# Performance work log

Measured on AMD Instinct MI355X. Metric: run time of the kernel, lower is better.

Reference implementation:

```python
import jax, jax.numpy as jnp
import numpy as np

B, R, C_M, C_Z, H, DH, NQP = 2, 384, 384, 128, 12, 32, 4
W_C = (2.0 / (9 * NQP)) ** (-0.5)   # (2/(9*n_qp))^-0.5
W_L = 3.0 ** 0.5                     # (1/3)^-0.5


def setup_inputs() -> dict:
    key = jax.random.key(0)
    ks = jax.random.split(key, 10)
    pair_rep = jax.random.normal(ks[0], (B, R, R, C_Z), jnp.float32)
    sing_rep = jax.random.normal(ks[1], (B, R, C_M), jnp.float32)
    m = jax.random.normal(ks[2], (B, R, 3, 3), jnp.float32)
    bbr, _ = jnp.linalg.qr(m)  # orthonormal backbone frames (B,R,3,3)
    bbt = jax.random.normal(ks[3], (B, R, 3), jnp.float32)
    s = 0.02
    W_qkv = jax.random.normal(ks[4], (C_M, DH * 3 * H), jnp.float32) * s
    W_qk = jax.random.normal(ks[5], (C_M, H * 2 * NQP * 3), jnp.float32) * s
    W_fc1 = jax.random.normal(ks[6], (C_Z, H), jnp.float32) * s
    b_fc1 = jnp.zeros((H,), jnp.float32)
    W0 = jax.random.normal(ks[7], (H * DH, C_M), jnp.float32) * s
    W1 = jax.random.normal(ks[8], (H * C_Z, C_M), jnp.float32) * s
    gamma = jax.random.uniform(ks[9], (1,), jnp.float32)
    return dict(pair_rep=pair_rep, sing_rep=sing_rep, bbr=bbr, bbt=bbt,
                W_qkv=W_qkv, W_qk=W_qk, W_fc1=W_fc1, b_fc1=b_fc1,
                W0=W0, W1=W1, gamma=gamma)


def reference(pair_rep, sing_rep, bbr, bbt, W_qkv, W_qk, W_fc1, b_fc1, W0, W1, gamma):
    # pair bias: fc1 then b i j h -> b h i j
    pair_bias = jnp.transpose(jnp.einsum('bijc,ch->bijh', pair_rep, W_fc1) + b_fc1,
                              (0, 3, 1, 2))                      # b h i j
    # scalar q/k/v: channel layout (dim_head, 3, heads)
    qkv = (sing_rep @ W_qkv).reshape(B, R, DH, 3, H)
    rq, rk, rv = (jnp.transpose(qkv[:, :, :, i, :], (0, 3, 1, 2)) for i in range(3))  # b h r d
    dot = jnp.einsum('bhid,bhjd->bhij', rq, rk) * DH ** (-0.5)
    # point q/k: channel layout (heads, 2, n_qp, 3)
    qk = (sing_rep @ W_qk).reshape(B, R, H, 2, NQP, 3)
    gq = jnp.transpose(qk[:, :, :, 0], (0, 3, 1, 2, 4))          # b p r h a
    gk = jnp.transpose(qk[:, :, :, 1], (0, 3, 1, 2, 4))
    # frame-transformed query/key points
    Tq = jnp.einsum('bprha,brak->phbrk', gq, bbr) + bbt          # p h b r 3
    Tk = jnp.einsum('bprha,brak->phbrk', gk, bbr) + bbt
    diff = Tq[:, :, :, :, None, :] - Tk[:, :, :, None, :, :]     # p h b i j 3
    sq = jnp.transpose(jnp.sum(diff * diff, axis=(0, -1)), (1, 0, 2, 3))  # b h i j
    head_w = jax.nn.softplus(gamma[0]) * W_C / 2                 # same scalar per head
    attn = jax.nn.softmax(W_L * (pair_bias + dot + head_w * sq), axis=-1)
    # pair-rep value aggregation -> W_1
    top = jnp.einsum('bhij,bijc->bihc', attn, pair_rep).reshape(B, R, H * C_Z) @ W1
    # scalar value aggregation -> W_0   (note: original adds these two only;
    # the point-value 'bot' branch is computed but unused in the output)
    out = jnp.transpose(jnp.einsum('bhij,bhjd->bhid', attn, rv),
                        (0, 2, 1, 3)).reshape(B, R, H * DH) @ W0
    return out + top
```

## Files before the change

kernel.cpp:

```cpp
#include <hip/hip_runtime.h>
#include <math.h>

#define Bb   2
#define Rr   384
#define CMd  384
#define CZ   128
#define Hh   12
#define DHd  32

#define WL           1.7320508075688772f
#define WC           4.242640687119285f
#define INV_SQRT_DH  0.17677669529663687f

#define SZ_R   (Bb*Hh*Rr*DHd)
#define SZ_T   (Bb*Hh*Rr*12)
#define SZ_S   (Bb*Hh*Rr)
#define SZ_A   ((long)Bb*Hh*Rr*Rr)
#define SZ_O   (Bb*Rr*Hh*DHd)

__global__ __launch_bounds__(64) void k_projgemm(
    const float* __restrict__ sing, const float* __restrict__ Wqkv,
    const float* __restrict__ Wqk, float* __restrict__ pbuf)
{
  const int t = threadIdx.x;
  const int m0 = blockIdx.x * 32;
  const int n0 = blockIdx.y * 32;
  const int ks = blockIdx.z;
  const int tx = t & 7, ty = t >> 3;
  __shared__ float As[32][36];
  __shared__ float Bs[32][36];
  float acc[4][4] = {};

  for (int kc = ks*192; kc < ks*192 + 192; kc += 32) {
    #pragma unroll
    for (int i = 0; i < 4; ++i) {
      int s = t + 64*i;
      int row = s >> 3, k4 = (s & 7) << 2;
      float4 v = *(const float4*)(sing + (long)(m0 + row)*384 + kc + k4);
      As[k4  ][row] = v.x; As[k4+1][row] = v.y;
      As[k4+2][row] = v.z; As[k4+3][row] = v.w;
    }
    #pragma unroll
    for (int i = 0; i < 4; ++i) {
      int s = t + 64*i;
      int k = s >> 3, c4 = (s & 7) << 2;
      const float* srcB = (n0 < 1152)
          ? Wqkv + (long)(kc + k)*1152 + n0 + c4
          : Wqk  + (long)(kc + k)*288 + (n0 - 1152) + c4;
      float4 w = *(const float4*)srcB;
      Bs[k][c4] = w.x; Bs[k][c4+1] = w.y; Bs[k][c4+2] = w.z; Bs[k][c4+3] = w.w;
    }
    __syncthreads();
    #pragma unroll
    for (int k = 0; k < 32; ++k) {
      float4 a = *(const float4*)&As[k][ty*4];
      float4 b = *(const float4*)&Bs[k][tx*4];
      acc[0][0] += a.x*b.x; acc[0][1] += a.x*b.y; acc[0][2] += a.x*b.z; acc[0][3] += a.x*b.w;
      acc[1][0] += a.y*b.x; acc[1][1] += a.y*b.y; acc[1][2] += a.y*b.z; acc[1][3] += a.y*b.w;
      acc[2][0] += a.z*b.x; acc[2][1] += a.z*b.y; acc[2][2] += a.z*b.z; acc[2][3] += a.z*b.w;
      acc[3][0] += a.w*b.x; acc[3][1] += a.w*b.y; acc[3][2] += a.w*b.z; acc[3][3] += a.w*b.w;
    }
    __syncthreads();
  }
  float* pd = pbuf + (long)ks * (768*1440);
  #pragma unroll
  for (int i = 0; i < 4; ++i)
    *(float4*)&pd[(long)(m0 + ty*4 + i)*1440 + n0 + tx*4] =
        make_float4(acc[i][0], acc[i][1], acc[i][2], acc[i][3]);
}

__global__ __launch_bounds__(256) void k_scatter(
    const float* __restrict__ pbuf,
    float* __restrict__ rq, float* __restrict__ rk, float* __restrict__ rv,
    float* __restrict__ gbuf)
{
  const int idx = blockIdx.x*256 + threadIdx.x;
  const int row = idx / 360;
  const int n   = (idx - row*360) * 4;
  float4 a = ((const float4*)pbuf)[idx];
  float4 b = ((const float4*)(pbuf + (long)768*1440))[idx];
  float v[4] = {a.x + b.x, a.y + b.y, a.z + b.z, a.w + b.w};
  const int bb = row / Rr, rr = row - bb*Rr;
  #pragma unroll
  for (int j = 0; j < 4; ++j) {
    int nj = n + j;
    if (nj < 1152) {
      int d = nj/36, rem = nj - d*36, wh = rem/12, h = rem - wh*12;
      float* dst = (wh == 0) ? rq : (wh == 1) ? rk : rv;
      dst[(((long)bb*Hh + h)*Rr + rr)*DHd + d] = v[j];
    } else {
      gbuf[(long)row*288 + nj - 1152] = v[j];
    }
  }
}

__global__ __launch_bounds__(256) void k_frame(
    const float* __restrict__ gbuf, const float* __restrict__ bbr,
    const float* __restrict__ bbt,
    float* __restrict__ TqF, float* __restrict__ TkF,
    float* __restrict__ Qsq, float* __restrict__ Ksq)
{
  const int idx = blockIdx.x*256 + threadIdx.x;
  const int row = idx / 24, q = idx - row*24;
  const int h = q >> 1, s2 = q & 1;
  const float* gp = gbuf + (long)row*288 + h*24 + s2*12;
  float rot[9], tr[3];
  #pragma unroll
  for (int a = 0; a < 9; ++a) rot[a] = bbr[(long)row*9 + a];
  #pragma unroll
  for (int a = 0; a < 3; ++a) tr[a] = bbt[(long)row*3 + a];
  const int b = row / Rr, r = row - b*Rr;
  float* T = s2 ? TkF : TqF;
  const long tb = (((long)b*Hh + h)*Rr + r)*12;
  float v[12]; float ss = 0.f;
  #pragma unroll
  for (int p = 0; p < 4; ++p)
    #pragma unroll
    for (int k2 = 0; k2 < 3; ++k2) {
      float x = gp[p*3+0]*rot[k2] + gp[p*3+1]*rot[3+k2] + gp[p*3+2]*rot[6+k2] + tr[k2];
      v[p*3+k2] = x; ss += x*x;
    }
  *(float4*)(T + tb)     = make_float4(v[0], v[1], v[2],  v[3]);
  *(float4*)(T + tb + 4) = make_float4(v[4], v[5], v[6],  v[7]);
  *(float4*)(T + tb + 8) = make_float4(v[8], v[9], v[10], v[11]);
  (s2 ? Ksq : Qsq)[((long)b*Hh + h)*Rr + r] = ss;
}

__global__ __launch_bounds__(256) void k_pbias(
    const float* __restrict__ pair, const float* __restrict__ Wfc1,
    const float* __restrict__ bfc1, float* __restrict__ pb)
{
  const int t = threadIdx.x;
  const int su = t & 7, rg = t >> 3;
  __shared__ __align__(16) float w_t[12*128];
  __shared__ float bias_l[12];
  for (int s = t; s < 1536; s += 256) {
    int h = s >> 7, c = s & 127;
    w_t[s] = Wfc1[c*12 + h];
  }
  if (t < 12) bias_l[t] = bfc1[t];
  __syncthreads();

  const long rbase = (long)blockIdx.x * 128;
  const float4* pr = (const float4*)pair;
  float acc[4][12] = {};
  #pragma unroll
  for (int cc = 0; cc < 4; ++cc) {
    const int f = su + 8*cc;
    float4 p0 = pr[(rbase + rg      )*32 + f];
    float4 p1 = pr[(rbase + rg + 32 )*32 + f];
    float4 p2 = pr[(rbase + rg + 64 )*32 + f];
    float4 p3 = pr[(rbase + rg + 96 )*32 + f];
    #pragma unroll
    for (int h = 0; h < 12; ++h) {
      float4 wv = *(const float4*)&w_t[h*128 + f*4];
      acc[0][h] += p0.x*wv.x + p0.y*wv.y + p0.z*wv.z + p0.w*wv.w;
      acc[1][h] += p1.x*wv.x + p1.y*wv.y + p1.z*wv.z + p1.w*wv.w;
      acc[2][h] += p2.x*wv.x + p2.y*wv.y + p2.z*wv.z + p2.w*wv.w;
      acc[3][h] += p3.x*wv.x + p3.y*wv.y + p3.z*wv.z + p3.w*wv.w;
    }
  }
  #pragma unroll
  for (int rr = 0; rr < 4; ++rr)
    #pragma unroll
    for (int h = 0; h < 12; ++h) {
      float v = acc[rr][h];
      v += __shfl_xor(v, 1, 64);
      v += __shfl_xor(v, 2, 64);
      v += __shfl_xor(v, 4, 64);
      acc[rr][h] = v;
    }
  if (su == 0) {
    const int b0 = (int)(rbase / 147456);
    const long ro = rbase - (long)b0*147456;
    #pragma unroll
    for (int rr = 0; rr < 4; ++rr) {
      const long jrow = ro + rg + 32*rr;
      #pragma unroll
      for (int h = 0; h < 12; ++h)
        pb[((long)b0*Hh + h)*147456 + jrow] = acc[rr][h] + bias_l[h];
    }
  }
}

#define ITILE 8
__global__ __launch_bounds__(256) void k_scores(
    const float* __restrict__ rq, const float* __restrict__ rk,
    const float* __restrict__ TqF, const float* __restrict__ TkF,
    const float* __restrict__ Qsq, const float* __restrict__ Ksq,
    const float* __restrict__ gamma, float* __restrict__ attn)
{
  const int t = threadIdx.x;
  const int nt = Rr / ITILE;
  const int bh = blockIdx.x / nt;
  const int i0 = (blockIdx.x - bh*nt) * ITILE;
  __shared__ float rk_l[384][33];
  __shared__ float rq_l[32];
  __shared__ float tq_l[12];
  __shared__ float scal[1];
  __shared__ float redm[4], reds[4];

  for (int idx = t; idx < 384*32; idx += 256)
    rk_l[idx >> 5][idx & 31] = rk[(long)bh*Rr*DHd + idx];

  const float g0 = gamma[0];
  const float head_w = log1pf(__expf(g0)) * (WC * 0.5f);

  for (int ii = 0; ii < ITILE; ++ii) {
    const int i = i0 + ii;
    if (t < 32) rq_l[t] = rq[((long)bh*Rr + i)*DHd + t];
    if (t < 12) tq_l[t] = TqF[((long)bh*Rr + i)*12 + t];
    if (t == 0) scal[0] = Qsq[(long)bh*Rr + i];
    __syncthreads();
    const float qs = scal[0];
    const long rowbase = ((long)bh*Rr + i)*Rr;

    auto logit_at = [&](int j) -> float {
      float dt = 0.f;
      #pragma unroll
      for (int dd = 0; dd < 32; ++dd) dt += rq_l[dd] * rk_l[j][dd];
      const float4* tk = (const float4*)(TkF + ((long)bh*Rr + j)*12);
      float4 ta = tk[0], tb = tk[1], tc = tk[2];
      float pt = tq_l[0]*ta.x + tq_l[1]*ta.y + tq_l[2]*ta.z + tq_l[3]*ta.w
               + tq_l[4]*tb.x + tq_l[5]*tb.y + tq_l[6]*tb.z + tq_l[7]*tb.w
               + tq_l[8]*tc.x + tq_l[9]*tc.y + tq_l[10]*tc.z + tq_l[11]*tc.w;
      float sqv = qs + Ksq[(long)bh*Rr + j] - 2.f*pt;
      return WL * (attn[rowbase + j] + dt*INV_SQRT_DH + head_w*sqv);
    };

    float l0 = logit_at(t);
    float l1 = (t < 128) ? logit_at(t + 256) : -3.4e38f;
    float m = fmaxf(l0, l1);
    #pragma unroll
    for (int s = 32; s; s >>= 1) m = fmaxf(m, __shfl_xor(m, s, 64));
    if ((t & 63) == 0) redm[t >> 6] = m;
    __syncthreads();
    m = fmaxf(fmaxf(redm[0], redm[1]), fmaxf(redm[2], redm[3]));
    float e0 = __expf(l0 - m);
    float e1 = (t < 128) ? __expf(l1 - m) : 0.f;
    float s = e0 + e1;
    #pragma unroll
    for (int sh = 32; sh; sh >>= 1) s += __shfl_xor(s, sh, 64);
    if ((t & 63) == 0) reds[t >> 6] = s;
    __syncthreads();
    float inv = 1.f / (reds[0] + reds[1] + reds[2] + reds[3]);
    attn[rowbase + t] = e0 * inv;
    if (t < 128) attn[rowbase + t + 256] = e1 * inv;
    __syncthreads();
  }
}

__global__ __launch_bounds__(256) void k_agg(
    const float* __restrict__ attn, const float* __restrict__ pair,
    const float* __restrict__ rv, float* __restrict__ o_ihd, float* __restrict__ top)
{
  const int t = threadIdx.x;
  const int bi = blockIdx.x;
  const int b = bi / Rr;
  const int i = bi - b*Rr;
  __shared__ float a_l[12][384];
  for (int idx = t; idx < 12*384; idx += 256) {
    int h = idx / 384, j = idx - h*384;
    a_l[h][j] = attn[(((long)b*Hh + h)*Rr + i)*Rr + j];
  }
  __syncthreads();
  const int c = t & 127, hh = t >> 7;
  const float* prow = pair + (long)bi * Rr * CZ;
  float acc0=0,acc1=0,acc2=0,acc3=0,acc4=0,acc5=0;
  for (int j = 0; j < 384; ++j) {
    float v = prow[(long)j*CZ + c];
    acc0 += a_l[hh   ][j]*v;
    acc1 += a_l[hh+2 ][j]*v;
    acc2 += a_l[hh+4 ][j]*v;
    acc3 += a_l[hh+6 ][j]*v;
    acc4 += a_l[hh+8 ][j]*v;
    acc5 += a_l[hh+10][j]*v;
  }
  float* tp = top + ((long)bi*Hh)*CZ + c;
  tp[(long)(hh   )*CZ] = acc0;
  tp[(long)(hh+2 )*CZ] = acc1;
  tp[(long)(hh+4 )*CZ] = acc2;
  tp[(long)(hh+6 )*CZ] = acc3;
  tp[(long)(hh+8 )*CZ] = acc4;
  tp[(long)(hh+10)*CZ] = acc5;
  for (int o = t; o < 384; o += 256) {
    int h = o >> 5, dd = o & 31;
    const float* rvp = rv + ((long)b*Hh + h)*Rr*DHd + dd;
    float s = 0.f;
    for (int j = 0; j < 384; ++j) s += a_l[h][j] * rvp[(long)j*DHd];
    o_ihd[(long)bi*384 + o] = s;
  }
}

#define K5_KSPLIT 6
#define K5_KLEN   320
__global__ __launch_bounds__(64) void k_final_part(
    const float* __restrict__ o_ihd, const float* __restrict__ top,
    const float* __restrict__ W0, const float* __restrict__ W1,
    float* __restrict__ partial)
{
  const int t = threadIdx.x;
  const int m0 = blockIdx.x * 32;
  const int n0 = blockIdx.y * 32;
  const int ks = blockIdx.z;
  const int tx = t & 7, ty = t >> 3;
  __shared__ float As[32][36];
  __shared__ float Bs[32][36];
  float acc[4][4] = {};

  for (int kc = ks*K5_KLEN; kc < ks*K5_KLEN + K5_KLEN; kc += 32) {
    #pragma unroll
    for (int i = 0; i < 4; ++i) {
      int s = t + 64*i;
      int row = s >> 3, k4 = (s & 7) << 2;
      int gk = kc + k4;
      const float* srcA = (gk < 384)
          ? o_ihd + (long)(m0 + row)*384 + gk
          : top   + (long)(m0 + row)*1536 + (gk - 384);
      float4 v = *(const float4*)srcA;
      As[k4  ][row] = v.x; As[k4+1][row] = v.y;
      As[k4+2][row] = v.z; As[k4+3][row] = v.w;
    }
    #pragma unroll
    for (int i = 0; i < 4; ++i) {
      int s = t + 64*i;
      int k = s >> 3, c4 = (s & 7) << 2;
      int gk = kc + k;
      const float* srcB = (gk < 384)
          ? W0 + (long)gk*384 + n0 + c4
          : W1 + (long)(gk - 384)*384 + n0 + c4;
      float4 w = *(const float4*)srcB;
      Bs[k][c4] = w.x; Bs[k][c4+1] = w.y; Bs[k][c4+2] = w.z; Bs[k][c4+3] = w.w;
    }
    __syncthreads();
    #pragma unroll
    for (int k = 0; k < 32; ++k) {
      float4 a = *(const float4*)&As[k][ty*4];
      float4 b = *(const float4*)&Bs[k][tx*4];
      acc[0][0] += a.x*b.x; acc[0][1] += a.x*b.y; acc[0][2] += a.x*b.z; acc[0][3] += a.x*b.w;
      acc[1][0] += a.y*b.x; acc[1][1] += a.y*b.y; acc[1][2] += a.y*b.z; acc[1][3] += a.y*b.w;
      acc[2][0] += a.z*b.x; acc[2][1] += a.z*b.y; acc[2][2] += a.z*b.z; acc[2][3] += a.z*b.w;
      acc[3][0] += a.w*b.x; acc[3][1] += a.w*b.y; acc[3][2] += a.w*b.z; acc[3][3] += a.w*b.w;
    }
    __syncthreads();
  }
  float* pdst = partial + (long)ks * (768*384);
  #pragma unroll
  for (int i = 0; i < 4; ++i)
    *(float4*)&pdst[(long)(m0 + ty*4 + i)*384 + n0 + tx*4] =
        make_float4(acc[i][0], acc[i][1], acc[i][2], acc[i][3]);
}

__global__ __launch_bounds__(256) void k_final_reduce(
    const float* __restrict__ partial, float* __restrict__ out)
{
  const int idx = blockIdx.x*256 + threadIdx.x;
  float4 r = make_float4(0.f, 0.f, 0.f, 0.f);
  #pragma unroll
  for (int p = 0; p < K5_KSPLIT; ++p) {
    float4 a = ((const float4*)(partial + (long)p*768*384))[idx];
    r.x += a.x; r.y += a.y; r.z += a.z; r.w += a.w;
  }
  ((float4*)out)[idx] = r;
}

extern "C" void kernel_launch(void* const* d_in, const int* in_sizes, int n_in,
                              void* d_out, int out_size, void* d_ws, size_t ws_size,
                              hipStream_t stream)
{
  (void)in_sizes; (void)n_in; (void)out_size; (void)ws_size;
  const float* pair  = (const float*)d_in[0];
  const float* sing  = (const float*)d_in[1];
  const float* bbr   = (const float*)d_in[2];
  const float* bbt   = (const float*)d_in[3];
  const float* Wqkv  = (const float*)d_in[4];
  const float* Wqk   = (const float*)d_in[5];
  const float* Wfc1  = (const float*)d_in[6];
  const float* bfc1  = (const float*)d_in[7];
  const float* W0    = (const float*)d_in[8];
  const float* W1    = (const float*)d_in[9];
  const float* gamma = (const float*)d_in[10];
  float* out = (float*)d_out;

  float* ws    = (float*)d_ws;
  float* rq    = ws;
  float* rk    = rq  + SZ_R;
  float* rv    = rk  + SZ_R;
  float* TqF   = rv  + SZ_R;
  float* TkF   = TqF + SZ_T;
  float* Qsq   = TkF + SZ_T;
  float* Ksq   = Qsq + SZ_S;
  float* attn  = Ksq + SZ_S;
  float* o_ihd = attn + SZ_A;
  float* top   = o_ihd + SZ_O;
  float* gbuf  = o_ihd;
  float* pbuf  = attn;
  float* partial = attn;

  k_projgemm<<<dim3(24, 45, 2), dim3(64), 0, stream>>>(sing, Wqkv, Wqk, pbuf);
  k_scatter<<<dim3(276480/256), dim3(256), 0, stream>>>(pbuf, rq, rk, rv, gbuf);
  k_frame<<<dim3(Bb*Rr*24/256), dim3(256), 0, stream>>>(
      gbuf, bbr, bbt, TqF, TkF, Qsq, Ksq);
  k_pbias<<<dim3(Bb*Rr*Rr/128), dim3(256), 0, stream>>>(pair, Wfc1, bfc1, attn);
  k_scores<<<dim3(Bb*Hh*(Rr/ITILE)), dim3(256), 0, stream>>>(
      rq, rk, TqF, TkF, Qsq, Ksq, gamma, attn);
  k_agg<<<dim3(Bb*Rr), dim3(256), 0, stream>>>(attn, pair, rv, o_ihd, top);
  k_final_part<<<dim3(24, 12, K5_KSPLIT), dim3(64), 0, stream>>>(
      o_ihd, top, W0, W1, partial);
  k_final_reduce<<<dim3(768*384/4/256), dim3(256), 0, stream>>>(partial, out);
}
```

Before: 192.9 us.

## Register-tile pair aggregation over all heads with float4 loads and tree reduction

Rewrites the pair-value aggregation in k_agg so each thread keeps a 12-head by 4-channel register tile and reads pair_rep with float4 loads. The key dimension is split across the 8 half-waves, and the partial sums are combined with a staged shared-memory reduction. Attention is stored transposed (j-major, padded to 20) so the 12 head weights load as three float4. The change aims to cut shared-memory traffic and per-FMA overhead, but it adds many barriers and about 48 accumulator registers. The scalar-value branch now reads attention straight from global memory instead of LDS.

Result: slower. 222.5 us (+15.4%).

```diff
diff --git a/kernel.cpp b/kernel.cpp
--- a/kernel.cpp
+++ b/kernel.cpp
@@ -258,36 +258,104 @@
   const int bi = blockIdx.x;
   const int b = bi / Rr;
   const int i = bi - b*Rr;
-  __shared__ float a_l[12][384];
-  for (int idx = t; idx < 12*384; idx += 256) {
+  const int w = t >> 6;
+  const int lane = t & 63;
+  const int jh = lane >> 5;
+  const int c4 = lane & 31;
+  __shared__ __align__(16) float attn_t[384*20];
+  __shared__ __align__(16) float4 red[2][12][32];
+
+  for (int idx = t; idx < 4608; idx += 256) {
     int h = idx / 384, j = idx - h*384;
-    a_l[h][j] = attn[(((long)b*Hh + h)*Rr + i)*Rr + j];
-  }
-  __syncthreads();
-  const int c = t & 127, hh = t >> 7;
-  const float* prow = pair + (long)bi * Rr * CZ;
-  float acc0=0,acc1=0,acc2=0,acc3=0,acc4=0,acc5=0;
-  for (int j = 0; j < 384; ++j) {
-    float v = prow[(long)j*CZ + c];
-    acc0 += a_l[hh   ][j]*v;
-    acc1 += a_l[hh+2 ][j]*v;
-    acc2 += a_l[hh+4 ][j]*v;
-    acc3 += a_l[hh+6 ][j]*v;
-    acc4 += a_l[hh+8 ][j]*v;
-    acc5 += a_l[hh+10][j]*v;
-  }
-  float* tp = top + ((long)bi*Hh)*CZ + c;
-  tp[(long)(hh   )*CZ] = acc0;
-  tp[(long)(hh+2 )*CZ] = acc1;
-  tp[(long)(hh+4 )*CZ] = acc2;
-  tp[(long)(hh+6 )*CZ] = acc3;
-  tp[(long)(hh+8 )*CZ] = acc4;
-  tp[(long)(hh+10)*CZ] = acc5;
+    attn_t[j*20 + h] = attn[(((long)b*Hh + h)*Rr + i)*Rr + j];
+  }
+  __syncthreads();
+
+  const float4* prow4 = (const float4*)(pair + (long)bi * Rr * CZ);
+  float4 acc[12];
+  #pragma unroll
+  for (int h = 0; h < 12; ++h) acc[h] = make_float4(0.f, 0.f, 0.f, 0.f);
+  #pragma unroll 4
+  for (int k = 0; k < 48; ++k) {
+    const int j = k*8 + w*2 + jh;
+    float4 pv  = prow4[j*32 + c4];
+    float4 av0 = *(const float4*)&attn_t[j*20 + 0];
+    float4 av1 = *(const float4*)&attn_t[j*20 + 4];
+    float4 av2 = *(const float4*)&attn_t[j*20 + 8];
+    acc[0].x += av0.x*pv.x; acc[0].y += av0.x*pv.y; acc[0].z += av0.x*pv.z; acc[0].w += av0.x*pv.w;
+    acc[1].x += av0.y*pv.x; acc[1].y += av0.y*pv.y; acc[1].z += av0.y*pv.z; acc[1].w += av0.y*pv.w;
+    acc[2].x += av0.z*pv.x; acc[2].y += av0.z*pv.y; acc[2].z += av0.z*pv.z; acc[2].w += av0.z*pv.w;
+    acc[3].x += av0.w*pv.x; acc[3].y += av0.w*pv.y; acc[3].z += av0.w*pv.z; acc[3].w += av0.w*pv.w;
+    acc[4].x += av1.x*pv.x; acc[4].y += av1.x*pv.y; acc[4].z += av1.x*pv.z; acc[4].w += av1.x*pv.w;
+    acc[5].x += av1.y*pv.x; acc[5].y += av1.y*pv.y; acc[5].z += av1.y*pv.z; acc[5].w += av1.y*pv.w;
+    acc[6].x += av1.z*pv.x; acc[6].y += av1.z*pv.y; acc[6].z += av1.z*pv.z; acc[6].w += av1.z*pv.w;
+    acc[7].x += av1.w*pv.x; acc[7].y += av1.w*pv.y; acc[7].z += av1.w*pv.z; acc[7].w += av1.w*pv.w;
+    acc[8].x += av2.x*pv.x; acc[8].y += av2.x*pv.y; acc[8].z += av2.x*pv.z; acc[8].w += av2.x*pv.w;
+    acc[9].x += av2.y*pv.x; acc[9].y += av2.y*pv.y; acc[9].z += av2.y*pv.z; acc[9].w += av2.y*pv.w;
+    acc[10].x += av2.z*pv.x; acc[10].y += av2.z*pv.y; acc[10].z += av2.z*pv.z; acc[10].w += av2.z*pv.w;
+    acc[11].x += av2.w*pv.x; acc[11].y += av2.w*pv.y; acc[11].z += av2.w*pv.z; acc[11].w += av2.w*pv.w;
+  }
+  __syncthreads();
+  if (w >= 2 && jh == 1) {
+    #pragma unroll
+    for (int h = 0; h < 12; ++h) red[w-2][h][c4] = acc[h];
+  }
+  __syncthreads();
+  if (w >= 2 && jh == 0) {
+    #pragma unroll
+    for (int h = 0; h < 12; ++h) {
+      float4 r = red[w-2][h][c4];
+      acc[h].x += r.x; acc[h].y += r.y; acc[h].z += r.z; acc[h].w += r.w;
+    }
+  }
+  __syncthreads();
+  if (w >= 2 && jh == 0) {
+    #pragma unroll
+    for (int h = 0; h < 12; ++h) red[w-2][h][c4] = acc[h];
+  }
+  __syncthreads();
+  if (w < 2 && jh == 0) {
+    #pragma unroll
+    for (int h = 0; h < 12; ++h) {
+      float4 r = red[w][h][c4];
+      acc[h].x += r.x; acc[h].y += r.y; acc[h].z += r.z; acc[h].w += r.w;
+    }
+  }
+  __syncthreads();
+  if (w < 2 && jh == 1) {
+    #pragma unroll
+    for (int h = 0; h < 12; ++h) red[w][h][c4] = acc[h];
+  }
+  __syncthreads();
+  if (w < 2 && jh == 0) {
+    #pragma unroll
+    for (int h = 0; h < 12; ++h) {
+      float4 r = red[w][h][c4];
+      acc[h].x += r.x; acc[h].y += r.y; acc[h].z += r.z; acc[h].w += r.w;
+    }
+  }
+  __syncthreads();
+  if (w == 1 && jh == 0) {
+    #pragma unroll
+    for (int h = 0; h < 12; ++h) red[0][h][c4] = acc[h];
+  }
+  __syncthreads();
+  if (w == 0 && jh == 0) {
+    #pragma unroll
+    for (int h = 0; h < 12; ++h) {
+      float4 r = red[0][h][c4];
+      acc[h].x += r.x; acc[h].y += r.y; acc[h].z += r.z; acc[h].w += r.w;
+      *(float4*)&top[((long)bi*Hh + h)*CZ + c4*4] = acc[h];
+    }
+  }
+
   for (int o = t; o < 384; o += 256) {
     int h = o >> 5, dd = o & 31;
+    const float* ap  = attn + (((long)b*Hh + h)*Rr + i)*Rr;
     const float* rvp = rv + ((long)b*Hh + h)*Rr*DHd + dd;
     float s = 0.f;
-    for (int j = 0; j < 384; ++j) s += a_l[h][j] * rvp[(long)j*DHd];
+    #pragma unroll 4
+    for (int j = 0; j < 384; ++j) s += ap[j] * rvp[(long)j*DHd];
     o_ihd[(long)bi*384 + o] = s;
   }
 }
```

## Fuse pair-bias projection with score computation and softmax per query row

Applied to the files above, without the earlier changes.

Merges the pair-bias kernel and the score/softmax kernel into one kernel with one block per (batch, query row). The block computes the 12-head pair bias for all j into shared memory, adds the scalar dot and point-distance terms, then runs softmax per head and writes attn once. This removes one full write and read of the B*H*R*R bias tensor in global memory and one launch. In exchange, rk and TkF are now read from global per row without shared-memory reuse across query rows, and the grid drops to 768 blocks.

Result: slower. 224.6 us (+16.5%).

```diff
diff --git a/kernel.cpp b/kernel.cpp
--- a/kernel.cpp
+++ b/kernel.cpp
@@ -126,127 +126,109 @@
   (s2 ? Ksq : Qsq)[((long)b*Hh + h)*Rr + r] = ss;
 }
 
-__global__ __launch_bounds__(256) void k_pbias(
+__global__ __launch_bounds__(256) void k_pscore(
     const float* __restrict__ pair, const float* __restrict__ Wfc1,
-    const float* __restrict__ bfc1, float* __restrict__ pb)
-{
-  const int t = threadIdx.x;
-  const int su = t & 7, rg = t >> 3;
-  __shared__ __align__(16) float w_t[12*128];
-  __shared__ float bias_l[12];
-  for (int s = t; s < 1536; s += 256) {
-    int h = s >> 7, c = s & 127;
-    w_t[s] = Wfc1[c*12 + h];
-  }
-  if (t < 12) bias_l[t] = bfc1[t];
-  __syncthreads();
-
-  const long rbase = (long)blockIdx.x * 128;
-  const float4* pr = (const float4*)pair;
-  float acc[4][12] = {};
-  #pragma unroll
-  for (int cc = 0; cc < 4; ++cc) {
-    const int f = su + 8*cc;
-    float4 p0 = pr[(rbase + rg      )*32 + f];
-    float4 p1 = pr[(rbase + rg + 32 )*32 + f];
-    float4 p2 = pr[(rbase + rg + 64 )*32 + f];
-    float4 p3 = pr[(rbase + rg + 96 )*32 + f];
-    #pragma unroll
-    for (int h = 0; h < 12; ++h) {
-      float4 wv = *(const float4*)&w_t[h*128 + f*4];
-      acc[0][h] += p0.x*wv.x + p0.y*wv.y + p0.z*wv.z + p0.w*wv.w;
-      acc[1][h] += p1.x*wv.x + p1.y*wv.y + p1.z*wv.z + p1.w*wv.w;
-      acc[2][h] += p2.x*wv.x + p2.y*wv.y + p2.z*wv.z + p2.w*wv.w;
-      acc[3][h] += p3.x*wv.x + p3.y*wv.y + p3.z*wv.z + p3.w*wv.w;
-    }
-  }
-  #pragma unroll
-  for (int rr = 0; rr < 4; ++rr)
-    #pragma unroll
-    for (int h = 0; h < 12; ++h) {
-      float v = acc[rr][h];
-      v += __shfl_xor(v, 1, 64);
-      v += __shfl_xor(v, 2, 64);
-      v += __shfl_xor(v, 4, 64);
-      acc[rr][h] = v;
-    }
-  if (su == 0) {
-    const int b0 = (int)(rbase / 147456);
-    const long ro = rbase - (long)b0*147456;
-    #pragma unroll
-    for (int rr = 0; rr < 4; ++rr) {
-      const long jrow = ro + rg + 32*rr;
-      #pragma unroll
-      for (int h = 0; h < 12; ++h)
-        pb[((long)b0*Hh + h)*147456 + jrow] = acc[rr][h] + bias_l[h];
-    }
-  }
-}
-
-#define ITILE 8
-__global__ __launch_bounds__(256) void k_scores(
+    const float* __restrict__ bfc1,
     const float* __restrict__ rq, const float* __restrict__ rk,
     const float* __restrict__ TqF, const float* __restrict__ TkF,
     const float* __restrict__ Qsq, const float* __restrict__ Ksq,
     const float* __restrict__ gamma, float* __restrict__ attn)
 {
   const int t = threadIdx.x;
-  const int nt = Rr / ITILE;
-  const int bh = blockIdx.x / nt;
-  const int i0 = (blockIdx.x - bh*nt) * ITILE;
-  __shared__ float rk_l[384][33];
-  __shared__ float rq_l[32];
-  __shared__ float tq_l[12];
-  __shared__ float scal[1];
-  __shared__ float redm[4], reds[4];
-
-  for (int idx = t; idx < 384*32; idx += 256)
-    rk_l[idx >> 5][idx & 31] = rk[(long)bh*Rr*DHd + idx];
-
-  const float g0 = gamma[0];
-  const float head_w = log1pf(__expf(g0)) * (WC * 0.5f);
-
-  for (int ii = 0; ii < ITILE; ++ii) {
-    const int i = i0 + ii;
-    if (t < 32) rq_l[t] = rq[((long)bh*Rr + i)*DHd + t];
-    if (t < 12) tq_l[t] = TqF[((long)bh*Rr + i)*12 + t];
-    if (t == 0) scal[0] = Qsq[(long)bh*Rr + i];
-    __syncthreads();
-    const float qs = scal[0];
-    const long rowbase = ((long)bh*Rr + i)*Rr;
-
-    auto logit_at = [&](int j) -> float {
-      float dt = 0.f;
-      #pragma unroll
-      for (int dd = 0; dd < 32; ++dd) dt += rq_l[dd] * rk_l[j][dd];
-      const float4* tk = (const float4*)(TkF + ((long)bh*Rr + j)*12);
-      float4 ta = tk[0], tb = tk[1], tc = tk[2];
-      float pt = tq_l[0]*ta.x + tq_l[1]*ta.y + tq_l[2]*ta.z + tq_l[3]*ta.w
-               + tq_l[4]*tb.x + tq_l[5]*tb.y + tq_l[6]*tb.z + tq_l[7]*tb.w
-               + tq_l[8]*tc.x + tq_l[9]*tc.y + tq_l[10]*tc.z + tq_l[11]*tc.w;
-      float sqv = qs + Ksq[(long)bh*Rr + j] - 2.f*pt;
-      return WL * (attn[rowbase + j] + dt*INV_SQRT_DH + head_w*sqv);
-    };
-
-    float l0 = logit_at(t);
-    float l1 = (t < 128) ? logit_at(t + 256) : -3.4e38f;
-    float m = fmaxf(l0, l1);
-    #pragma unroll
-    for (int s = 32; s; s >>= 1) m = fmaxf(m, __shfl_xor(m, s, 64));
-    if ((t & 63) == 0) redm[t >> 6] = m;
-    __syncthreads();
-    m = fmaxf(fmaxf(redm[0], redm[1]), fmaxf(redm[2], redm[3]));
-    float e0 = __expf(l0 - m);
-    float e1 = (t < 128) ? __expf(l1 - m) : 0.f;
-    float s = e0 + e1;
-    #pragma unroll
-    for (int sh = 32; sh; sh >>= 1) s += __shfl_xor(s, sh, 64);
-    if ((t & 63) == 0) reds[t >> 6] = s;
-    __syncthreads();
-    float inv = 1.f / (reds[0] + reds[1] + reds[2] + reds[3]);
-    attn[rowbase + t] = e0 * inv;
-    if (t < 128) attn[rowbase + t + 256] = e1 * inv;
-    __syncthreads();
+  const int bi = blockIdx.x;
+  const int b = bi / Rr;
+  const int i = bi - b*Rr;
+  __shared__ __align__(16) float w_t[12*128];
+  __shared__ float attn_l[12][388];
+  __shared__ __align__(16) float rq_l[12][32];
+  __shared__ float tq_l[12][12];
+  __shared__ float bias_l[12], qs_l[12];
+
+  for (int s = t; s < 1536; s += 256) {
+    int h = s >> 7, c = s & 127;
+    w_t[s] = Wfc1[c*12 + h];
+  }
+  for (int s = t; s < 384; s += 256) {
+    int h = s >> 5, d = s & 31;
+    rq_l[h][d] = rq[(((long)b*Hh + h)*Rr + i)*DHd + d];
+  }
+  if (t < 144) tq_l[t/12][t%12] = TqF[(((long)b*Hh + t/12)*Rr + i)*12 + t%12];
+  if (t < 12) { bias_l[t] = bfc1[t]; qs_l[t] = Qsq[((long)b*Hh + t)*Rr + i]; }
+  const float head_w = log1pf(__expf(gamma[0])) * (WC * 0.5f);
+  __syncthreads();
+
+  {
+    const int su = t & 7, rg = t >> 3;
+    const float4* pr = (const float4*)(pair + (long)bi * Rr * CZ);
+    for (int k = 0; k < 12; ++k) {
+      const int j = k*32 + rg;
+      float acc[12] = {};
+      #pragma unroll
+      for (int cc = 0; cc < 4; ++cc) {
+        const int f = su + 8*cc;
+        float4 p = pr[(long)j*32 + f];
+        #pragma unroll
+        for (int h = 0; h < 12; ++h) {
+          float4 wv = *(const float4*)&w_t[h*128 + f*4];
+          acc[h] += p.x*wv.x + p.y*wv.y + p.z*wv.z + p.w*wv.w;
+        }
+      }
+      #pragma unroll
+      for (int h = 0; h < 12; ++h) {
+        float v = acc[h];
+        v += __shfl_xor(v, 1, 64);
+        v += __shfl_xor(v, 2, 64);
+        v += __shfl_xor(v, 4, 64);
+        if (su == 0) attn_l[h][j] = v + bias_l[h];
+      }
+    }
+  }
+  __syncthreads();
+
+  for (int k = 0; k < 18; ++k) {
+    int tid = t + 256*k;
+    int h = tid / 384, j = tid - h*384;
+    const long rbase = ((long)b*Hh + h)*Rr + j;
+    const float4* kp = (const float4*)(rk + rbase*DHd);
+    float dt = 0.f;
+    #pragma unroll
+    for (int q4 = 0; q4 < 8; ++q4) {
+      float4 v = kp[q4];
+      dt += rq_l[h][q4*4]*v.x + rq_l[h][q4*4+1]*v.y + rq_l[h][q4*4+2]*v.z + rq_l[h][q4*4+3]*v.w;
+    }
+    const float4* tk = (const float4*)(TkF + rbase*12);
+    float4 ta = tk[0], tb2 = tk[1], tc = tk[2];
+    float pt = tq_l[h][0]*ta.x + tq_l[h][1]*ta.y + tq_l[h][2]*ta.z + tq_l[h][3]*ta.w
+             + tq_l[h][4]*tb2.x + tq_l[h][5]*tb2.y + tq_l[h][6]*tb2.z + tq_l[h][7]*tb2.w
+             + tq_l[h][8]*tc.x + tq_l[h][9]*tc.y + tq_l[h][10]*tc.z + tq_l[h][11]*tc.w;
+    float sq = qs_l[h] + Ksq[rbase] - 2.f*pt;
+    attn_l[h][j] = WL * (attn_l[h][j] + dt*INV_SQRT_DH + head_w*sq);
+  }
+  __syncthreads();
+
+  {
+    const int w = t >> 6, lane = t & 63;
+    #pragma unroll
+    for (int r = 0; r < 3; ++r) {
+      const int h = w + 4*r;
+      float x[6];
+      #pragma unroll
+      for (int k = 0; k < 6; ++k) x[k] = attn_l[h][lane + 64*k];
+      float m = x[0];
+      #pragma unroll
+      for (int k = 1; k < 6; ++k) m = fmaxf(m, x[k]);
+      #pragma unroll
+      for (int s = 32; s; s >>= 1) m = fmaxf(m, __shfl_xor(m, s, 64));
+      float sum = 0.f;
+      #pragma unroll
+      for (int k = 0; k < 6; ++k) { x[k] = __expf(x[k] - m); sum += x[k]; }
+      #pragma unroll
+      for (int s = 32; s; s >>= 1) sum += __shfl_xor(sum, s, 64);
+      const float inv = 1.f / sum;
+      float* arow = attn + (((long)b*Hh + h)*Rr + i)*Rr;
+      #pragma unroll
+      for (int k = 0; k < 6; ++k) arow[lane + 64*k] = x[k] * inv;
+    }
   }
 }
 
@@ -401,9 +383,8 @@
   k_scatter<<<dim3(276480/256), dim3(256), 0, stream>>>(pbuf, rq, rk, rv, gbuf);
   k_frame<<<dim3(Bb*Rr*24/256), dim3(256), 0, stream>>>(
       gbuf, bbr, bbt, TqF, TkF, Qsq, Ksq);
-  k_pbias<<<dim3(Bb*Rr*Rr/128), dim3(256), 0, stream>>>(pair, Wfc1, bfc1, attn);
-  k_scores<<<dim3(Bb*Hh*(Rr/ITILE)), dim3(256), 0, stream>>>(
-      rq, rk, TqF, TkF, Qsq, Ksq, gamma, attn);
+  k_pscore<<<dim3(Bb*Rr), dim3(256), 0, stream>>>(
+      pair, Wfc1, bfc1, rq, rk, TqF, TkF, Qsq, Ksq, gamma, attn);
   k_agg<<<dim3(Bb*Rr), dim3(256), 0, stream>>>(attn, pair, rv, o_ihd, top);
   k_final_part<<<dim3(24, 12, K5_KSPLIT), dim3(64), 0, stream>>>(
       o_ihd, top, W0, W1, partial);
```
